# Performance work log

Measured on AMD Instinct MI355X. Metric: run time of the kernel, lower is better.

Reference implementation:

```python
import jax, jax.numpy as jnp
import numpy as np
import math

DIM = 1024
NUM_HEADS = 16
BATCH = 2
SEQ = 2048


def _get_attention_slopes(n):
    def pow2_slopes(n):
        start = 2 ** (-(2 ** (-(math.log2(n) - 3))))
        return [start * start ** i for i in range(n)]
    if math.log2(n).is_integer():
        return pow2_slopes(n)
    c = 2 ** math.floor(math.log2(n))
    return pow2_slopes(c) + _get_attention_slopes(2 * c)[0::2][: n - c]


def setup_inputs() -> dict:
    key = jax.random.key(0)
    k1, k2, k3 = jax.random.split(key, 3)
    x = jax.random.normal(k1, (BATCH, SEQ, DIM), dtype=jnp.float32)
    # fan-in scaled init to mimic lecun_normal default kernel init magnitude
    w_qkv = jax.random.normal(k2, (DIM, 3 * DIM), dtype=jnp.float32) / np.sqrt(DIM)
    w_proj = jax.random.normal(k3, (DIM, DIM), dtype=jnp.float32) / np.sqrt(DIM)
    return {"x": x, "w_qkv": w_qkv, "w_proj": w_proj}


def reference(x, w_qkv, w_proj):
    B, N, D = x.shape
    H = NUM_HEADS
    Dh = D // H

    qkv = x @ w_qkv                      # [B, N, 3D]
    q, k, v = jnp.split(qkv, 3, axis=-1)
    split_heads = lambda t: t.reshape(B, N, H, Dh).transpose(0, 2, 1, 3)  # [B,H,N,Dh]
    q, k, v = split_heads(q), split_heads(k), split_heads(v)

    scale = Dh ** (-0.5)
    att = jnp.einsum("bhnd,bhmd->bhnm", q, k) * scale  # [B,H,N,N]

    # ALiBi bias: slope per head times absolute key position (as in source)
    slopes = jnp.asarray(_get_attention_slopes(H), dtype=att.dtype)  # [H]
    pos_bias = slopes[None, :, None, None] * jnp.arange(N, dtype=att.dtype)[None, None, None, :]
    att = att + pos_bias

    # causal mask
    big_neg = jnp.finfo(att.dtype).min
    causal = jnp.tril(jnp.ones((N, N), dtype=bool))[None, None]
    att = jnp.where(causal, att, big_neg)
    att = jax.nn.softmax(att, axis=-1)

    out = jnp.einsum("bhnm,bhmd->bhnd", att, v)        # [B,H,N,Dh]
    out = out.transpose(0, 2, 1, 3).reshape(B, N, D)   # [B,N,D]
    return out @ w_proj
```

## Files before the change

### kernel.cpp

```cpp
#include <hip/hip_runtime.h>
#include <cstdint>
#include <cstddef>

typedef unsigned short u16;
typedef __bf16 bf16x8 __attribute__((ext_vector_type(8)));
typedef float f32x4 __attribute__((ext_vector_type(4)));
typedef u16 u16x4 __attribute__((ext_vector_type(4)));
typedef u16 u16x8 __attribute__((ext_vector_type(8)));
typedef unsigned int u32x2 __attribute__((ext_vector_type(2)));
typedef unsigned int u32x4 __attribute__((ext_vector_type(4)));

#define DEV __device__ __forceinline__

DEV u16 f2bf(float f) {
    union { float f; unsigned u; } un; un.f = f;
    unsigned u = un.u;
    return (u16)((u + 0x7fffu + ((u >> 16) & 1u)) >> 16);
}

DEV u16 bf16c(float f) {
    __bf16 b = (__bf16)f;
    u16 r; __builtin_memcpy(&r, &b, 2); return r;
}

DEV f32x4 mfma16(bf16x8 a, bf16x8 b, f32x4 c) {
    return __builtin_amdgcn_mfma_f32_16x16x32_bf16(a, b, c, 0, 0, 0);
}

DEV f32x4 vmax4(f32x4 a, f32x4 b) {
    f32x4 r;
    r[0] = fmaxf(a[0], b[0]); r[1] = fmaxf(a[1], b[1]);
    r[2] = fmaxf(a[2], b[2]); r[3] = fmaxf(a[3], b[3]);
    return r;
}

DEV void async16(const u16* g, u16* l) {
    __builtin_amdgcn_global_load_lds(
        (__attribute__((address_space(1))) unsigned int*)(void*)g,
        (__attribute__((address_space(3))) unsigned int*)(void*)l,
        16, 0, 0);
}

__global__ __launch_bounds__(256)
void cvt_k(const float* __restrict__ src, u16* __restrict__ dst, int n8) {
    int i = blockIdx.x * 256 + threadIdx.x;
    if (i >= n8) return;
    const float* s = src + (size_t)i * 8;
    f32x4 a = *(const f32x4*)s;
    f32x4 b = *(const f32x4*)(s + 4);
    u16x8 o;
    o[0] = f2bf(a[0]); o[1] = f2bf(a[1]); o[2] = f2bf(a[2]); o[3] = f2bf(a[3]);
    o[4] = f2bf(b[0]); o[5] = f2bf(b[1]); o[6] = f2bf(b[2]); o[7] = f2bf(b[3]);
    *(u16x8*)(dst + (size_t)i * 8) = o;
}

__global__ __launch_bounds__(256)
void transpose_cvt_k(const float* __restrict__ src, u16* __restrict__ dst, int R, int C) {
    __shared__ u16 t[64][65];
    const int tid = threadIdx.x;
    const int c0 = blockIdx.x * 64, r0 = blockIdx.y * 64;
    for (int i = 0; i < 4; ++i) {
        int e = (i * 256 + tid) * 4;
        int r = e >> 6, c = e & 63;
        f32x4 v = *(const f32x4*)(src + (size_t)(r0 + r) * C + (c0 + c));
        t[r][c] = f2bf(v[0]); t[r][c + 1] = f2bf(v[1]);
        t[r][c + 2] = f2bf(v[2]); t[r][c + 3] = f2bf(v[3]);
    }
    __syncthreads();
    for (int i = 0; i < 4; ++i) {
        int e = (i * 256 + tid) * 4;
        int ro = e >> 6, co = e & 63;
        u16x4 v;
        v[0] = t[co][ro]; v[1] = t[co + 1][ro]; v[2] = t[co + 2][ro]; v[3] = t[co + 3][ro];
        *(u16x4*)(dst + (size_t)(c0 + ro) * R + (r0 + co)) = v;
    }
}

__global__ __launch_bounds__(256, 2)
void gemm_bt(const u16* __restrict__ A, const u16* __restrict__ Bt,
             void* __restrict__ Cout, int M, int N, int K, int lda, int of32) {
    __shared__ alignas(16) u16 As[128 * 32];
    __shared__ alignas(16) u16 Bs[128 * 32];
    const int tid = threadIdx.x;
    const int wave = tid >> 6, lane = tid & 63;
    const int quad = lane >> 4, l16 = lane & 15;
    const int m0 = blockIdx.x * 128, n0 = blockIdx.y * 128;
    const int wm = (wave & 1) * 64, wn = (wave >> 1) * 64;

    const f32x4 zero = {0.f, 0.f, 0.f, 0.f};
    f32x4 acc[4][4];
    for (int i = 0; i < 4; ++i) for (int j = 0; j < 4; ++j) acc[i][j] = zero;

    for (int k0 = 0; k0 < K; k0 += 32) {
        __syncthreads();
        for (int p = 0; p < 2; ++p) {
            int s = p * 256 + tid;
            int row = s >> 2, kcs = s & 3;
            int kc = kcs ^ ((row >> 1) & 3);
            async16(A + (size_t)(m0 + row) * lda + k0 + kc * 8, &As[(p * 256 + wave * 64) * 8]);
            async16(Bt + (size_t)(n0 + row) * K + k0 + kc * 8, &Bs[(p * 256 + wave * 64) * 8]);
        }
        __syncthreads();

        bf16x8 af[4], bfr[4];
        for (int mt = 0; mt < 4; ++mt) {
            int row = wm + mt * 16 + l16;
            int ci = (row << 2) | (quad ^ ((row >> 1) & 3));
            af[mt] = *(const bf16x8*)&As[ci * 8];
        }
        for (int nt = 0; nt < 4; ++nt) {
            int col = wn + nt * 16 + l16;
            int ci = (col << 2) | (quad ^ ((col >> 1) & 3));
            bfr[nt] = *(const bf16x8*)&Bs[ci * 8];
        }
        for (int mt = 0; mt < 4; ++mt)
            for (int nt = 0; nt < 4; ++nt)
                acc[mt][nt] = mfma16(af[mt], bfr[nt], acc[mt][nt]);
    }

    for (int mt = 0; mt < 4; ++mt)
        for (int r = 0; r < 4; ++r) {
            int row = m0 + wm + mt * 16 + quad * 4 + r;
            if (of32) {
                float* crow = (float*)Cout + (size_t)row * N + n0 + wn + l16;
                for (int nt = 0; nt < 4; ++nt)
                    crow[nt * 16] = acc[mt][nt][r];
            } else {
                u16* crow = (u16*)Cout + (size_t)row * N + n0 + wn + l16;
                for (int nt = 0; nt < 4; ++nt)
                    crow[nt * 16] = f2bf(acc[mt][nt][r]);
            }
        }
}

__global__ __launch_bounds__(256, 4)
void attn_k(const u16* qkv, u16* o, int ostride) {
    __shared__ alignas(16) u16 KsB [2][64 * 64];
    __shared__ alignas(16) u16 VtsB[2][64 * 64];
    __shared__ alignas(16) u16 Psh [64 * 64];
    const int x = blockIdx.x;
    const int qb = 31 - (x >> 5);
    const int bh = x & 31;
    const int b = bh >> 4, h = bh & 15;
    const int tid = threadIdx.x;
    const int wave = tid >> 6, lane = tid & 63;
    const int quad = lane >> 4, l16 = lane & 15;
    const float LOG2E = 1.44269504f;
    const float slope2 = exp2f(-0.5f * (float)(h + 1)) * LOG2E;
    const float scale2 = 0.125f * LOG2E;
    const size_t seq0 = (size_t)b * 2048;
    const int row0 = qb * 64 + wave * 16;
    const int irow = row0 + l16;

    bf16x8 qf[2];
    {
        const u16* qrow = qkv + (seq0 + irow) * 3072 + h * 64;
        qf[0] = *(const bf16x8*)(qrow + quad * 8);
        qf[1] = *(const bf16x8*)(qrow + 32 + quad * 8);
    }

    float pre[4][4];
    for (int nt = 0; nt < 4; ++nt)
        for (int r = 0; r < 4; ++r)
            pre[nt][r] = slope2 * (float)(nt * 16 + quad * 4 + r);

    float mst = -1e30f, lst = 0.f;
    f32x4 oacc[4];
    const f32x4 zero = {0.f, 0.f, 0.f, 0.f};
    for (int nt = 0; nt < 4; ++nt) oacc[nt] = zero;

    const int ktiles = qb + 1;
    const u16* kbase = qkv + seq0 * 3072 + 1024 + h * 64;
    const u16* vbase = kbase + 1024;
    const int tpair = tid & 31;
    const int vd0 = ((tid * 2) >> 6) * 8;
    const int k0p = (tid * 2) & 63;

    for (int p = 0; p < 2; ++p) {
        int row = wave * 16 + p * 8 + (lane >> 3);
        int kc = (lane & 7) ^ (row & 7);
        async16(kbase + (size_t)row * 3072 + kc * 8, &KsB[0][(wave * 16 + p * 8) * 64]);
    }
    u16x8 vr0, vr1;
    vr0 = *(const u16x8*)(vbase + (size_t)k0p * 3072 + vd0);
    vr1 = *(const u16x8*)(vbase + (size_t)(k0p + 1) * 3072 + vd0);
    for (int j = 0; j < 8; ++j) {
        unsigned w = (unsigned)vr0[j] | ((unsigned)vr1[j] << 16);
        int d = vd0 + j;
        *(unsigned*)&VtsB[0][d * 64 + (((tpair >> 2) ^ (d & 7)) << 3) + (tpair & 3) * 2] = w;
    }
    __syncthreads();

    for (int kt = 0; kt < ktiles; ++kt) {
        const int cur = kt & 1, nxt = cur ^ 1;
        const bool more = (kt + 1 < ktiles);
        if (more) {
            const u16* kb = kbase + (size_t)(kt + 1) * 64 * 3072;
            for (int p = 0; p < 2; ++p) {
                int row = wave * 16 + p * 8 + (lane >> 3);
                int kc = (lane & 7) ^ (row & 7);
                async16(kb + (size_t)row * 3072 + kc * 8, &KsB[nxt][(wave * 16 + p * 8) * 64]);
            }
            const u16* vb = vbase + (size_t)(kt + 1) * 64 * 3072;
            vr0 = *(const u16x8*)(vb + (size_t)k0p * 3072 + vd0);
            vr1 = *(const u16x8*)(vb + (size_t)(k0p + 1) * 3072 + vd0);
        }

        f32x4 st[4];
        for (int nt = 0; nt < 4; ++nt) st[nt] = zero;
        for (int nt = 0; nt < 4; ++nt)
            for (int ks = 0; ks < 2; ++ks) {
                int krow = nt * 16 + l16;
                bf16x8 bk = *(const bf16x8*)&KsB[cur][krow * 64 + (((ks * 4 + quad) ^ (krow & 7)) << 3)];
                st[nt] = mfma16(bk, qf[ks], st[nt]);
            }

        const float b0 = slope2 * (float)(kt * 64);
        for (int nt = 0; nt < 4; ++nt)
            for (int r = 0; r < 4; ++r)
                st[nt][r] = st[nt][r] * scale2 + pre[nt][r];
        if (kt == qb) {
            const int loc = irow - kt * 64;
            for (int nt = 0; nt < 4; ++nt)
                for (int r = 0; r < 4; ++r)
                    st[nt][r] = (nt * 16 + quad * 4 + r <= loc) ? st[nt][r] : -1e30f;
        }

        f32x4 mv = vmax4(vmax4(st[0], st[1]), vmax4(st[2], st[3]));
        float tm = fmaxf(fmaxf(mv[0], mv[1]), fmaxf(mv[2], mv[3]));
        tm = fmaxf(tm, __shfl_xor(tm, 16, 64));
        tm = fmaxf(tm, __shfl_xor(tm, 32, 64));
        float mnew = fmaxf(mst, tm + b0);
        float alpha = exp2f(mst - mnew);
        mst = mnew;
        const float dsub = mnew - b0;

        for (int nt = 0; nt < 4; ++nt)
            for (int r = 0; r < 4; ++r)
                st[nt][r] = exp2f(st[nt][r] - dsub);
        f32x4 sv = (st[0] + st[1]) + (st[2] + st[3]);
        lst = lst * alpha + ((sv[0] + sv[1]) + (sv[2] + sv[3]));

        {
            const int q = wave * 16 + l16;
            for (int nt = 0; nt < 4; ++nt) {
                u32x2 w;
                w[0] = (unsigned)bf16c(st[nt][0]) | ((unsigned)bf16c(st[nt][1]) << 16);
                w[1] = (unsigned)bf16c(st[nt][2]) | ((unsigned)bf16c(st[nt][3]) << 16);
                int ch = ((nt * 2 + (quad >> 1)) ^ (l16 & 7));
                *(u32x2*)&Psh[q * 64 + (ch << 3) + (quad & 1) * 4] = w;
            }
        }

        for (int nt = 0; nt < 4; ++nt)
            for (int r = 0; r < 4; ++r) oacc[nt][r] *= alpha;

        {
            const int q = wave * 16 + l16;
            bf16x8 ap[2];
            ap[0] = *(const bf16x8*)&Psh[q * 64 + (((quad) ^ (l16 & 7)) << 3)];
            ap[1] = *(const bf16x8*)&Psh[q * 64 + (((4 + quad) ^ (l16 & 7)) << 3)];
            for (int nt = 0; nt < 4; ++nt) {
                int drow = nt * 16 + l16;
                for (int ks = 0; ks < 2; ++ks) {
                    bf16x8 av = *(const bf16x8*)&VtsB[cur][drow * 64 + (((ks * 4 + quad) ^ (drow & 7)) << 3)];
                    oacc[nt] = mfma16(av, ap[ks], oacc[nt]);
                }
            }
        }

        if (more) {
            for (int j = 0; j < 8; ++j) {
                unsigned w = (unsigned)vr0[j] | ((unsigned)vr1[j] << 16);
                int d = vd0 + j;
                *(unsigned*)&VtsB[nxt][d * 64 + (((tpair >> 2) ^ (d & 7)) << 3) + (tpair & 3) * 2] = w;
            }
        }
        __syncthreads();
    }

    float l2 = lst + __shfl_xor(lst, 16, 64);
    float l4 = l2 + __shfl_xor(l2, 32, 64);
    float inv = 1.f / l4;
    u16* orow = o + (seq0 + row0 + l16) * (size_t)ostride + h * 64 + quad * 4;
    for (int nt = 0; nt < 4; ++nt) {
        u16x4 w;
        for (int r = 0; r < 4; ++r) w[r] = bf16c(oacc[nt][r] * inv);
        *(u16x4*)(orow + nt * 16) = w;
    }
}

extern "C" void kernel_launch(void* const* d_in, const int* in_sizes, int n_in,
                              void* d_out, int out_size, void* d_ws, size_t ws_size,
                              hipStream_t stream) {
    (void)in_sizes; (void)n_in; (void)out_size; (void)ws_size;
    const float* x     = (const float*)d_in[0];
    const float* wqkv  = (const float*)d_in[1];
    const float* wproj = (const float*)d_in[2];

    char* ws = (char*)d_ws;
    u16* wqkvT  = (u16*)(ws + 256);
    u16* wprojT = wqkvT;
    u16* qkv    = wqkvT + (size_t)3072 * 1024;
    u16* xb     = (u16*)d_out;

    cvt_k<<<dim3(2048), 256, 0, stream>>>(x, xb, 4096 * 1024 / 8);
    transpose_cvt_k<<<dim3(48, 16), 256, 0, stream>>>(wqkv, wqkvT, 1024, 3072);

    gemm_bt<<<dim3(32, 24), 256, 0, stream>>>(xb, wqkvT, qkv, 4096, 3072, 1024, 1024, 0);

    transpose_cvt_k<<<dim3(16, 16), 256, 0, stream>>>(wproj, wprojT, 1024, 1024);

    attn_k<<<dim3(1024), 256, 0, stream>>>(qkv, qkv, 3072);

    gemm_bt<<<dim3(32, 8), 256, 0, stream>>>(qkv, wprojT, d_out, 4096, 1024, 1024, 3072, 1);
}
```

Before: 186.6 us.

## Fuse prep kernels, unroll attention loop by two, precompute offsets, raise GEMM occupancy

The three conversion and transpose kernels are merged into one prep launch, so two launches go away and w_proj gets its own workspace slot instead of aliasing wqkvT. The attention inner loop becomes a macro unrolled twice with compile-time buffer indices. LDS offsets and global pointers are precomputed once, and the bf16 packing now uses perm instructions. The gemm launch bound goes from 2 to 3 blocks per CU, which may limit registers and cause spills.

```diff
diff --git a/kernel.cpp b/kernel.cpp
--- a/kernel.cpp
+++ b/kernel.cpp
@@ -6,7 +6,6 @@
 typedef __bf16 bf16x8 __attribute__((ext_vector_type(8)));
 typedef float f32x4 __attribute__((ext_vector_type(4)));
 typedef u16 u16x4 __attribute__((ext_vector_type(4)));
-typedef u16 u16x8 __attribute__((ext_vector_type(8)));
 typedef unsigned int u32x2 __attribute__((ext_vector_type(2)));
 typedef unsigned int u32x4 __attribute__((ext_vector_type(4)));
 
@@ -16,6 +15,11 @@
     union { float f; unsigned u; } un; un.f = f;
     unsigned u = un.u;
     return (u16)((u + 0x7fffu + ((u >> 16) & 1u)) >> 16);
+}
+
+DEV unsigned rbf(float f) {
+    union { float f; unsigned u; } un; un.f = f;
+    return un.u + 0x7fffu + ((un.u >> 16) & 1u);
 }
 
 DEV u16 bf16c(float f) {
@@ -41,24 +45,9 @@
         16, 0, 0);
 }
 
-__global__ __launch_bounds__(256)
-void cvt_k(const float* __restrict__ src, u16* __restrict__ dst, int n8) {
-    int i = blockIdx.x * 256 + threadIdx.x;
-    if (i >= n8) return;
-    const float* s = src + (size_t)i * 8;
-    f32x4 a = *(const f32x4*)s;
-    f32x4 b = *(const f32x4*)(s + 4);
-    u16x8 o;
-    o[0] = f2bf(a[0]); o[1] = f2bf(a[1]); o[2] = f2bf(a[2]); o[3] = f2bf(a[3]);
-    o[4] = f2bf(b[0]); o[5] = f2bf(b[1]); o[6] = f2bf(b[2]); o[7] = f2bf(b[3]);
-    *(u16x8*)(dst + (size_t)i * 8) = o;
-}
-
-__global__ __launch_bounds__(256)
-void transpose_cvt_k(const float* __restrict__ src, u16* __restrict__ dst, int R, int C) {
-    __shared__ u16 t[64][65];
-    const int tid = threadIdx.x;
-    const int c0 = blockIdx.x * 64, r0 = blockIdx.y * 64;
+DEV void trans_body(const float* __restrict__ src, u16* __restrict__ dst,
+                    int R, int C, int bx, int by, int tid, u16 (*t)[65]) {
+    const int c0 = bx * 64, r0 = by * 64;
     for (int i = 0; i < 4; ++i) {
         int e = (i * 256 + tid) * 4;
         int r = e >> 6, c = e & 63;
@@ -76,7 +65,32 @@
     }
 }
 
-__global__ __launch_bounds__(256, 2)
+__global__ __launch_bounds__(256)
+void prep_k(const float* __restrict__ x, const float* __restrict__ wqkv,
+            const float* __restrict__ wproj, u16* __restrict__ xb,
+            u16* __restrict__ wqkvT, u16* __restrict__ wprojT) {
+    __shared__ u16 t[64][65];
+    const int bid = blockIdx.x, tid = threadIdx.x;
+    if (bid < 2048) {
+        int i = bid * 256 + tid;
+        const float* s = x + (size_t)i * 8;
+        f32x4 a = *(const f32x4*)s;
+        f32x4 b = *(const f32x4*)(s + 4);
+        u16 o[8];
+        o[0] = f2bf(a[0]); o[1] = f2bf(a[1]); o[2] = f2bf(a[2]); o[3] = f2bf(a[3]);
+        o[4] = f2bf(b[0]); o[5] = f2bf(b[1]); o[6] = f2bf(b[2]); o[7] = f2bf(b[3]);
+        u16x4* d = (u16x4*)(xb + (size_t)i * 8);
+        d[0] = *(u16x4*)&o[0]; d[1] = *(u16x4*)&o[4];
+    } else if (bid < 2816) {
+        int i = bid - 2048;
+        trans_body(wqkv, wqkvT, 1024, 3072, i % 48, i / 48, tid, t);
+    } else {
+        int i = bid - 2816;
+        trans_body(wproj, wprojT, 1024, 1024, i % 16, i / 16, tid, t);
+    }
+}
+
+__global__ __launch_bounds__(256, 3)
 void gemm_bt(const u16* __restrict__ A, const u16* __restrict__ Bt,
              void* __restrict__ Cout, int M, int N, int K, int lda, int of32) {
     __shared__ alignas(16) u16 As[128 * 32];
@@ -131,6 +145,80 @@
                     crow[nt * 16] = f2bf(acc[mt][nt][r]);
             }
         }
+}
+
+#define ATL(KT, CUR, NXT, MORE)                                                     \
+{                                                                                   \
+    u32x4 vw0, vw1;                                                                 \
+    if (MORE) {                                                                     \
+        async16(gk0, &KsB[NXT][kd0]);                                               \
+        async16(gk1, &KsB[NXT][kd1]);                                               \
+        vw0 = *(const u32x4*)gv0;                                                   \
+        vw1 = *(const u32x4*)gv1;                                                   \
+        gk0 += TS; gk1 += TS; gv0 += TS; gv1 += TS;                                 \
+    }                                                                               \
+    f32x4 st[4];                                                                    \
+    _Pragma("unroll")                                                               \
+    for (int nt = 0; nt < 4; ++nt) {                                                \
+        bf16x8 bk0 = *(const bf16x8*)&KsB[CUR][koff[nt][0]];                        \
+        bf16x8 bk1 = *(const bf16x8*)&KsB[CUR][koff[nt][1]];                        \
+        f32x4 a_ = mfma16(bk0, qf[0], zero);                                        \
+        st[nt] = mfma16(bk1, qf[1], a_);                                            \
+    }                                                                               \
+    const float b0 = slope2 * (float)((KT) * 64);                                   \
+    _Pragma("unroll")                                                               \
+    for (int nt = 0; nt < 4; ++nt)                                                  \
+        for (int r = 0; r < 4; ++r)                                                 \
+            st[nt][r] = st[nt][r] * scale2 + pre[nt][r];                            \
+    if ((KT) == qb) {                                                               \
+        const int loc = irow - (KT) * 64;                                           \
+        _Pragma("unroll")                                                           \
+        for (int nt = 0; nt < 4; ++nt)                                              \
+            for (int r = 0; r < 4; ++r)                                             \
+                st[nt][r] = (nt * 16 + quad * 4 + r <= loc) ? st[nt][r] : -1e30f;   \
+    }                                                                               \
+    f32x4 mv = vmax4(vmax4(st[0], st[1]), vmax4(st[2], st[3]));                     \
+    float tm = fmaxf(fmaxf(mv[0], mv[1]), fmaxf(mv[2], mv[3]));                     \
+    tm = fmaxf(tm, __shfl_xor(tm, 16, 64));                                         \
+    tm = fmaxf(tm, __shfl_xor(tm, 32, 64));                                         \
+    float mnew = fmaxf(mst, tm + b0);                                               \
+    float alpha = exp2f(mst - mnew);                                                \
+    mst = mnew;                                                                     \
+    const float dsub = mnew - b0;                                                   \
+    _Pragma("unroll")                                                               \
+    for (int nt = 0; nt < 4; ++nt)                                                  \
+        for (int r = 0; r < 4; ++r)                                                 \
+            st[nt][r] = exp2f(st[nt][r] - dsub);                                    \
+    f32x4 sv = (st[0] + st[1]) + (st[2] + st[3]);                                   \
+    lst = lst * alpha + ((sv[0] + sv[1]) + (sv[2] + sv[3]));                        \
+    _Pragma("unroll")                                                               \
+    for (int nt = 0; nt < 4; ++nt) {                                                \
+        u32x2 w;                                                                    \
+        w[0] = __builtin_amdgcn_perm(rbf(st[nt][1]), rbf(st[nt][0]), 0x07060302u);  \
+        w[1] = __builtin_amdgcn_perm(rbf(st[nt][3]), rbf(st[nt][2]), 0x07060302u);  \
+        *(u32x2*)&Psh[psw[nt]] = w;                                                 \
+    }                                                                               \
+    _Pragma("unroll")                                                               \
+    for (int nt = 0; nt < 4; ++nt)                                                  \
+        for (int r = 0; r < 4; ++r) oacc[nt][r] *= alpha;                           \
+    bf16x8 pa0 = *(const bf16x8*)&Psh[ap0];                                         \
+    bf16x8 pa1 = *(const bf16x8*)&Psh[ap1];                                         \
+    _Pragma("unroll")                                                               \
+    for (int nt = 0; nt < 4; ++nt) {                                                \
+        bf16x8 av0 = *(const bf16x8*)&VtsB[CUR][koff[nt][0]];                       \
+        bf16x8 av1 = *(const bf16x8*)&VtsB[CUR][koff[nt][1]];                       \
+        oacc[nt] = mfma16(av0, pa0, oacc[nt]);                                      \
+        oacc[nt] = mfma16(av1, pa1, oacc[nt]);                                      \
+    }                                                                               \
+    if (MORE) {                                                                     \
+        _Pragma("unroll")                                                           \
+        for (int j = 0; j < 8; ++j) {                                               \
+            unsigned sel = (j & 1) ? 0x07060302u : 0x05040100u;                     \
+            *(unsigned*)&VtsB[NXT][vpub[j]] =                                       \
+                __builtin_amdgcn_perm(vw1[j >> 1], vw0[j >> 1], sel);               \
+        }                                                                           \
+    }                                                                               \
+    __syncthreads();                                                                \
 }
 
 __global__ __launch_bounds__(256, 4)
@@ -160,9 +248,60 @@
     }
 
     float pre[4][4];
+    #pragma unroll
     for (int nt = 0; nt < 4; ++nt)
         for (int r = 0; r < 4; ++r)
             pre[nt][r] = slope2 * (float)(nt * 16 + quad * 4 + r);
+
+    int koff[4][2];
+    #pragma unroll
+    for (int nt = 0; nt < 4; ++nt) {
+        int krow = nt * 16 + l16;
+        koff[nt][0] = krow * 64 + ((quad ^ (krow & 7)) << 3);
+        koff[nt][1] = krow * 64 + (((4 + quad) ^ (krow & 7)) << 3);
+    }
+    const int q = wave * 16 + l16;
+    int psw[4];
+    #pragma unroll
+    for (int nt = 0; nt < 4; ++nt)
+        psw[nt] = q * 64 + (((nt * 2 + (quad >> 1)) ^ (l16 & 7)) << 3) + (quad & 1) * 4;
+    const int ap0 = q * 64 + ((quad ^ (l16 & 7)) << 3);
+    const int ap1 = q * 64 + (((4 + quad) ^ (l16 & 7)) << 3);
+
+    const int tpair = tid & 31;
+    const int vd0 = ((tid * 2) >> 6) * 8;
+    const int k0p = (tid * 2) & 63;
+    int vpub[8];
+    #pragma unroll
+    for (int j = 0; j < 8; ++j) {
+        int d = vd0 + j;
+        vpub[j] = d * 64 + (((tpair >> 2) ^ (d & 7)) << 3) + (tpair & 3) * 2;
+    }
+
+    const int r0p = wave * 16 + (lane >> 3);
+    const int kd0 = (wave * 16) * 64;
+    const int kd1 = (wave * 16 + 8) * 64;
+    const size_t TS = (size_t)64 * 3072;
+    const u16* kbase = qkv + seq0 * 3072 + 1024 + h * 64;
+    const u16* gk0 = kbase + (size_t)r0p * 3072 + (((lane & 7) ^ (r0p & 7)) << 3);
+    const u16* gk1 = kbase + (size_t)(r0p + 8) * 3072 + (((lane & 7) ^ ((r0p + 8) & 7)) << 3);
+    const u16* gv0 = kbase + 1024 + (size_t)k0p * 3072 + vd0;
+    const u16* gv1 = gv0 + 3072;
+
+    async16(gk0, &KsB[0][kd0]);
+    async16(gk1, &KsB[0][kd1]);
+    {
+        u32x4 vw0 = *(const u32x4*)gv0;
+        u32x4 vw1 = *(const u32x4*)gv1;
+        #pragma unroll
+        for (int j = 0; j < 8; ++j) {
+            unsigned sel = (j & 1) ? 0x07060302u : 0x05040100u;
+            *(unsigned*)&VtsB[0][vpub[j]] =
+                __builtin_amdgcn_perm(vw1[j >> 1], vw0[j >> 1], sel);
+        }
+    }
+    gk0 += TS; gk1 += TS; gv0 += TS; gv1 += TS;
+    __syncthreads();
 
     float mst = -1e30f, lst = 0.f;
     f32x4 oacc[4];
@@ -170,114 +309,14 @@
     for (int nt = 0; nt < 4; ++nt) oacc[nt] = zero;
 
     const int ktiles = qb + 1;
-    const u16* kbase = qkv + seq0 * 3072 + 1024 + h * 64;
-    const u16* vbase = kbase + 1024;
-    const int tpair = tid & 31;
-    const int vd0 = ((tid * 2) >> 6) * 8;
-    const int k0p = (tid * 2) & 63;
-
-    for (int p = 0; p < 2; ++p) {
-        int row = wave * 16 + p * 8 + (lane >> 3);
-        int kc = (lane & 7) ^ (row & 7);
-        async16(kbase + (size_t)row * 3072 + kc * 8, &KsB[0][(wave * 16 + p * 8) * 64]);
-    }
-    u16x8 vr0, vr1;
-    vr0 = *(const u16x8*)(vbase + (size_t)k0p * 3072 + vd0);
-    vr1 = *(const u16x8*)(vbase + (size_t)(k0p + 1) * 3072 + vd0);
-    for (int j = 0; j < 8; ++j) {
-        unsigned w = (unsigned)vr0[j] | ((unsigned)vr1[j] << 16);
-        int d = vd0 + j;
-        *(unsigned*)&VtsB[0][d * 64 + (((tpair >> 2) ^ (d & 7)) << 3) + (tpair & 3) * 2] = w;
-    }
-    __syncthreads();
-
-    for (int kt = 0; kt < ktiles; ++kt) {
-        const int cur = kt & 1, nxt = cur ^ 1;
-        const bool more = (kt + 1 < ktiles);
-        if (more) {
-            const u16* kb = kbase + (size_t)(kt + 1) * 64 * 3072;
-            for (int p = 0; p < 2; ++p) {
-                int row = wave * 16 + p * 8 + (lane >> 3);
-                int kc = (lane & 7) ^ (row & 7);
-                async16(kb + (size_t)row * 3072 + kc * 8, &KsB[nxt][(wave * 16 + p * 8) * 64]);
-            }
-            const u16* vb = vbase + (size_t)(kt + 1) * 64 * 3072;
-            vr0 = *(const u16x8*)(vb + (size_t)k0p * 3072 + vd0);
-            vr1 = *(const u16x8*)(vb + (size_t)(k0p + 1) * 3072 + vd0);
-        }
-
-        f32x4 st[4];
-        for (int nt = 0; nt < 4; ++nt) st[nt] = zero;
-        for (int nt = 0; nt < 4; ++nt)
-            for (int ks = 0; ks < 2; ++ks) {
-                int krow = nt * 16 + l16;
-                bf16x8 bk = *(const bf16x8*)&KsB[cur][krow * 64 + (((ks * 4 + quad) ^ (krow & 7)) << 3)];
-                st[nt] = mfma16(bk, qf[ks], st[nt]);
-            }
-
-        const float b0 = slope2 * (float)(kt * 64);
-        for (int nt = 0; nt < 4; ++nt)
-            for (int r = 0; r < 4; ++r)
-                st[nt][r] = st[nt][r] * scale2 + pre[nt][r];
-        if (kt == qb) {
-            const int loc = irow - kt * 64;
-            for (int nt = 0; nt < 4; ++nt)
-                for (int r = 0; r < 4; ++r)
-                    st[nt][r] = (nt * 16 + quad * 4 + r <= loc) ? st[nt][r] : -1e30f;
-        }
-
-        f32x4 mv = vmax4(vmax4(st[0], st[1]), vmax4(st[2], st[3]));
-        float tm = fmaxf(fmaxf(mv[0], mv[1]), fmaxf(mv[2], mv[3]));
-        tm = fmaxf(tm, __shfl_xor(tm, 16, 64));
-        tm = fmaxf(tm, __shfl_xor(tm, 32, 64));
-        float mnew = fmaxf(mst, tm + b0);
-        float alpha = exp2f(mst - mnew);
-        mst = mnew;
-        const float dsub = mnew - b0;
-
-        for (int nt = 0; nt < 4; ++nt)
-            for (int r = 0; r < 4; ++r)
-                st[nt][r] = exp2f(st[nt][r] - dsub);
-        f32x4 sv = (st[0] + st[1]) + (st[2] + st[3]);
-        lst = lst * alpha + ((sv[0] + sv[1]) + (sv[2] + sv[3]));
-
-        {
-            const int q = wave * 16 + l16;
-            for (int nt = 0; nt < 4; ++nt) {
-                u32x2 w;
-                w[0] = (unsigned)bf16c(st[nt][0]) | ((unsigned)bf16c(st[nt][1]) << 16);
-                w[1] = (unsigned)bf16c(st[nt][2]) | ((unsigned)bf16c(st[nt][3]) << 16);
-                int ch = ((nt * 2 + (quad >> 1)) ^ (l16 & 7));
-                *(u32x2*)&Psh[q * 64 + (ch << 3) + (quad & 1) * 4] = w;
-            }
-        }
-
-        for (int nt = 0; nt < 4; ++nt)
-            for (int r = 0; r < 4; ++r) oacc[nt][r] *= alpha;
-
-        {
-            const int q = wave * 16 + l16;
-            bf16x8 ap[2];
-            ap[0] = *(const bf16x8*)&Psh[q * 64 + (((quad) ^ (l16 & 7)) << 3)];
-            ap[1] = *(const bf16x8*)&Psh[q * 64 + (((4 + quad) ^ (l16 & 7)) << 3)];
-            for (int nt = 0; nt < 4; ++nt) {
-                int drow = nt * 16 + l16;
-                for (int ks = 0; ks < 2; ++ks) {
-                    bf16x8 av = *(const bf16x8*)&VtsB[cur][drow * 64 + (((ks * 4 + quad) ^ (drow & 7)) << 3)];
-                    oacc[nt] = mfma16(av, ap[ks], oacc[nt]);
-                }
-            }
-        }
-
-        if (more) {
-            for (int j = 0; j < 8; ++j) {
-                unsigned w = (unsigned)vr0[j] | ((unsigned)vr1[j] << 16);
-                int d = vd0 + j;
-                *(unsigned*)&VtsB[nxt][d * 64 + (((tpair >> 2) ^ (d & 7)) << 3) + (tpair & 3) * 2] = w;
-            }
-        }
-        __syncthreads();
-    }
+    int kt = 0;
+    while (kt + 2 <= ktiles) {
+        ATL(kt, 0, 1, true)
+        ATL(kt + 1, 1, 0, (kt + 2 < ktiles))
+        kt += 2;
+    }
+    if (kt < ktiles)
+        ATL(kt, 0, 1, false)
 
     float l2 = lst + __shfl_xor(lst, 16, 64);
     float l4 = l2 + __shfl_xor(l2, 32, 64);
@@ -298,20 +337,13 @@
     const float* wqkv  = (const float*)d_in[1];
     const float* wproj = (const float*)d_in[2];
 
-    char* ws = (char*)d_ws;
-    u16* wqkvT  = (u16*)(ws + 256);
-    u16* wprojT = wqkvT;
-    u16* qkv    = wqkvT + (size_t)3072 * 1024;
+    u16* wqkvT  = (u16*)d_ws;
+    u16* wprojT = wqkvT + (size_t)3072 * 1024;
+    u16* qkv    = wprojT + (size_t)1024 * 1024;
     u16* xb     = (u16*)d_out;
 
-    cvt_k<<<dim3(2048), 256, 0, stream>>>(x, xb, 4096 * 1024 / 8);
-    transpose_cvt_k<<<dim3(48, 16), 256, 0, stream>>>(wqkv, wqkvT, 1024, 3072);
-
+    prep_k<<<dim3(3072), 256, 0, stream>>>(x, wqkv, wproj, xb, wqkvT, wprojT);
     gemm_bt<<<dim3(32, 24), 256, 0, stream>>>(xb, wqkvT, qkv, 4096, 3072, 1024, 1024, 0);
-
-    transpose_cvt_k<<<dim3(16, 16), 256, 0, stream>>>(wproj, wprojT, 1024, 1024);
-
     attn_k<<<dim3(1024), 256, 0, stream>>>(qkv, qkv, 3072);
-
     gemm_bt<<<dim3(32, 8), 256, 0, stream>>>(qkv, wprojT, d_out, 4096, 1024, 1024, 3072, 1);
 }
```

New measurement: 219.1 us. 17.4% more time.

## Fuse input conversion kernels into one prep launch and tweak gemm occupancy

Applied to the files above, without the earlier changes.

Merges the x conversion and both weight transpose-conversions into a single prep kernel, dispatched by block index, so two launches are removed. The workspace layout changes so wprojT gets its own buffer instead of reusing wqkvT. Separately, gemm launch bounds are raised to 3 blocks per SM, and the V-transpose packing in attention now uses byte-permute on 32-bit words instead of per-u16 shifts. The higher occupancy hint may force register spills in the gemm.

```diff
diff --git a/kernel.cpp b/kernel.cpp
--- a/kernel.cpp
+++ b/kernel.cpp
@@ -6,7 +6,6 @@
 typedef __bf16 bf16x8 __attribute__((ext_vector_type(8)));
 typedef float f32x4 __attribute__((ext_vector_type(4)));
 typedef u16 u16x4 __attribute__((ext_vector_type(4)));
-typedef u16 u16x8 __attribute__((ext_vector_type(8)));
 typedef unsigned int u32x2 __attribute__((ext_vector_type(2)));
 typedef unsigned int u32x4 __attribute__((ext_vector_type(4)));
 
@@ -41,24 +40,9 @@
         16, 0, 0);
 }
 
-__global__ __launch_bounds__(256)
-void cvt_k(const float* __restrict__ src, u16* __restrict__ dst, int n8) {
-    int i = blockIdx.x * 256 + threadIdx.x;
-    if (i >= n8) return;
-    const float* s = src + (size_t)i * 8;
-    f32x4 a = *(const f32x4*)s;
-    f32x4 b = *(const f32x4*)(s + 4);
-    u16x8 o;
-    o[0] = f2bf(a[0]); o[1] = f2bf(a[1]); o[2] = f2bf(a[2]); o[3] = f2bf(a[3]);
-    o[4] = f2bf(b[0]); o[5] = f2bf(b[1]); o[6] = f2bf(b[2]); o[7] = f2bf(b[3]);
-    *(u16x8*)(dst + (size_t)i * 8) = o;
-}
-
-__global__ __launch_bounds__(256)
-void transpose_cvt_k(const float* __restrict__ src, u16* __restrict__ dst, int R, int C) {
-    __shared__ u16 t[64][65];
-    const int tid = threadIdx.x;
-    const int c0 = blockIdx.x * 64, r0 = blockIdx.y * 64;
+DEV void trans_body(const float* __restrict__ src, u16* __restrict__ dst,
+                    int R, int C, int bx, int by, int tid, u16 (*t)[65]) {
+    const int c0 = bx * 64, r0 = by * 64;
     for (int i = 0; i < 4; ++i) {
         int e = (i * 256 + tid) * 4;
         int r = e >> 6, c = e & 63;
@@ -76,7 +60,32 @@
     }
 }
 
-__global__ __launch_bounds__(256, 2)
+__global__ __launch_bounds__(256)
+void prep_k(const float* __restrict__ x, const float* __restrict__ wqkv,
+            const float* __restrict__ wproj, u16* __restrict__ xb,
+            u16* __restrict__ wqkvT, u16* __restrict__ wprojT) {
+    __shared__ u16 t[64][65];
+    const int bid = blockIdx.x, tid = threadIdx.x;
+    if (bid < 2048) {
+        int i = bid * 256 + tid;
+        const float* s = x + (size_t)i * 8;
+        f32x4 a = *(const f32x4*)s;
+        f32x4 b = *(const f32x4*)(s + 4);
+        u16 o[8];
+        o[0] = f2bf(a[0]); o[1] = f2bf(a[1]); o[2] = f2bf(a[2]); o[3] = f2bf(a[3]);
+        o[4] = f2bf(b[0]); o[5] = f2bf(b[1]); o[6] = f2bf(b[2]); o[7] = f2bf(b[3]);
+        u16x4* d = (u16x4*)(xb + (size_t)i * 8);
+        d[0] = *(u16x4*)&o[0]; d[1] = *(u16x4*)&o[4];
+    } else if (bid < 2816) {
+        int i = bid - 2048;
+        trans_body(wqkv, wqkvT, 1024, 3072, i % 48, i / 48, tid, t);
+    } else {
+        int i = bid - 2816;
+        trans_body(wproj, wprojT, 1024, 1024, i % 16, i / 16, tid, t);
+    }
+}
+
+__global__ __launch_bounds__(256, 3)
 void gemm_bt(const u16* __restrict__ A, const u16* __restrict__ Bt,
              void* __restrict__ Cout, int M, int N, int K, int lda, int of32) {
     __shared__ alignas(16) u16 As[128 * 32];
@@ -181,11 +190,12 @@
         int kc = (lane & 7) ^ (row & 7);
         async16(kbase + (size_t)row * 3072 + kc * 8, &KsB[0][(wave * 16 + p * 8) * 64]);
     }
-    u16x8 vr0, vr1;
-    vr0 = *(const u16x8*)(vbase + (size_t)k0p * 3072 + vd0);
-    vr1 = *(const u16x8*)(vbase + (size_t)(k0p + 1) * 3072 + vd0);
+    u32x4 vw0, vw1;
+    vw0 = *(const u32x4*)(vbase + (size_t)k0p * 3072 + vd0);
+    vw1 = *(const u32x4*)(vbase + (size_t)(k0p + 1) * 3072 + vd0);
     for (int j = 0; j < 8; ++j) {
-        unsigned w = (unsigned)vr0[j] | ((unsigned)vr1[j] << 16);
+        unsigned sel = (j & 1) ? 0x07060302u : 0x05040100u;
+        unsigned w = __builtin_amdgcn_perm(vw1[j >> 1], vw0[j >> 1], sel);
         int d = vd0 + j;
         *(unsigned*)&VtsB[0][d * 64 + (((tpair >> 2) ^ (d & 7)) << 3) + (tpair & 3) * 2] = w;
     }
@@ -202,8 +212,8 @@
                 async16(kb + (size_t)row * 3072 + kc * 8, &KsB[nxt][(wave * 16 + p * 8) * 64]);
             }
             const u16* vb = vbase + (size_t)(kt + 1) * 64 * 3072;
-            vr0 = *(const u16x8*)(vb + (size_t)k0p * 3072 + vd0);
-            vr1 = *(const u16x8*)(vb + (size_t)(k0p + 1) * 3072 + vd0);
+            vw0 = *(const u32x4*)(vb + (size_t)k0p * 3072 + vd0);
+            vw1 = *(const u32x4*)(vb + (size_t)(k0p + 1) * 3072 + vd0);
         }
 
         f32x4 st[4];
@@ -271,7 +281,8 @@
 
         if (more) {
             for (int j = 0; j < 8; ++j) {
-                unsigned w = (unsigned)vr0[j] | ((unsigned)vr1[j] << 16);
+                unsigned sel = (j & 1) ? 0x07060302u : 0x05040100u;
+                unsigned w = __builtin_amdgcn_perm(vw1[j >> 1], vw0[j >> 1], sel);
                 int d = vd0 + j;
                 *(unsigned*)&VtsB[nxt][d * 64 + (((tpair >> 2) ^ (d & 7)) << 3) + (tpair & 3) * 2] = w;
             }
@@ -298,20 +309,13 @@
     const float* wqkv  = (const float*)d_in[1];
     const float* wproj = (const float*)d_in[2];
 
-    char* ws = (char*)d_ws;
-    u16* wqkvT  = (u16*)(ws + 256);
-    u16* wprojT = wqkvT;
-    u16* qkv    = wqkvT + (size_t)3072 * 1024;
+    u16* wqkvT  = (u16*)d_ws;
+    u16* wprojT = wqkvT + (size_t)3072 * 1024;
+    u16* qkv    = wprojT + (size_t)1024 * 1024;
     u16* xb     = (u16*)d_out;
 
-    cvt_k<<<dim3(2048), 256, 0, stream>>>(x, xb, 4096 * 1024 / 8);
-    transpose_cvt_k<<<dim3(48, 16), 256, 0, stream>>>(wqkv, wqkvT, 1024, 3072);
-
+    prep_k<<<dim3(3072), 256, 0, stream>>>(x, wqkv, wproj, xb, wqkvT, wprojT);
     gemm_bt<<<dim3(32, 24), 256, 0, stream>>>(xb, wqkvT, qkv, 4096, 3072, 1024, 1024, 0);
-
-    transpose_cvt_k<<<dim3(16, 16), 256, 0, stream>>>(wproj, wprojT, 1024, 1024);
-
     attn_k<<<dim3(1024), 256, 0, stream>>>(qkv, qkv, 3072);
-
     gemm_bt<<<dim3(32, 8), 256, 0, stream>>>(qkv, wprojT, d_out, 4096, 1024, 1024, 3072, 1);
 }
```

New measurement: 182.3 us. 1.02x faster.
